# Kernel optimization log

Measured on AMD Instinct MI355X. Metric: run time of the kernel, lower is better.

Reference implementation:

```python
import jax, jax.numpy as jnp
import numpy as np

COMMITMENT_LOSS_WEIGHT = 0.25


def setup_inputs() -> dict:
    key = jax.random.key(0)
    k1, k2 = jax.random.split(key)
    B, H, W, C = 64, 32, 32, 256
    D, K = H * W, 1024  # embedding_dim = H*W per the rearrange+reshape in call()
    x = jax.random.normal(k1, (B, H, W, C), dtype=jnp.float32)
    # Orthogonal initializer (like tf.keras.initializers.Orthogonal) via QR
    E = jnp.linalg.qr(jax.random.normal(k2, (D, K), dtype=jnp.float32))[0]
    return {"x": x, "embeddings": E.astype(jnp.float32)}


def reference(x, embeddings):
    B, H, W, C = x.shape
    D = H * W  # embedding_dim
    # einops: 'b h w c -> b c (h w)'
    cont = jnp.transpose(x, (0, 3, 1, 2)).reshape(B, C, D)
    flat = cont.reshape(-1, D)  # [B*C, D]
    # squared L2 distances via norm + matmul (as in get_discretised)
    dists = (jnp.sum(flat * flat, axis=1, keepdims=True)
             + jnp.sum(embeddings * embeddings, axis=0)
             - 2.0 * (flat @ embeddings))  # [B*C, K]
    idx = jnp.argmin(dists, axis=1)  # [B*C]
    # one_hot @ embeddings.T == direct gather of codebook columns
    quantised = embeddings.T[idx].reshape(B, C, D)
    codebook_loss = jnp.mean((jax.lax.stop_gradient(cont) - quantised) ** 2)
    commitment_loss = COMMITMENT_LOSS_WEIGHT * jnp.mean(
        (cont - jax.lax.stop_gradient(quantised)) ** 2)
    loss = codebook_loss + commitment_loss  # layer add_loss terms, summed
    # einops: 'b c (h w) -> b h w c'
    q_bhwc = jnp.transpose(quantised.reshape(B, C, H, W), (0, 2, 3, 1))
    discretised = idx.reshape(-1, C)  # [B, C]
    # straight-through estimator
    q_out = x + jax.lax.stop_gradient(q_bhwc - x)
    return q_out, discretised, loss
```

## Files before the change

kernel.cpp:

```cpp
#include <hip/hip_runtime.h>
#include <float.h>
#include <stdint.h>

#define B_   64
#define C_   256
#define D_   1024
#define K_   1024
#define M_   16384
#define NX_  16777216
#define DISC_OFF NX_
#define LOSS_OFF (NX_ + M_)

typedef _Float16 h8 __attribute__((ext_vector_type(8)));
typedef float    f4 __attribute__((ext_vector_type(4)));

#define XSCALE 512.0f
#define ESCALE 2048.0f
#define DOT_UNSCALE_2 (2.0f / 1048576.0f)

#define WS_EH  0
#define WS_EL  524288
#define WS_CN  1048576
#define WS_PCN 1049600
#define WS_PV  1049600
#define WS_PI  1180672

__device__ __forceinline__ void async16(const _Float16* g, _Float16* l) {
    __builtin_amdgcn_global_load_lds(
        (const __attribute__((address_space(1))) unsigned int*)g,
        (__attribute__((address_space(3))) unsigned int*)l, 16, 0, 0);
}

__global__ __launch_bounds__(256) void split_kernel(const float* __restrict__ x,
                                                    const float* __restrict__ E,
                                                    _Float16* __restrict__ Xh,
                                                    _Float16* __restrict__ Xl,
                                                    _Float16* __restrict__ Eh,
                                                    _Float16* __restrict__ El,
                                                    float* __restrict__ pcn) {
    const int bid = blockIdx.x;
    if (bid < 512) {
        const int tid = bid * 256 + threadIdx.x;
        const int n   = tid & 1023;
        const int o   = tid >> 10;
        const int d0  = o * 8;
        h8 hh, ll;
        float s = 0.f;
        #pragma unroll
        for (int i = 0; i < 8; ++i) {
            const float v = E[(size_t)(d0 + i) * K_ + n];
            s = fmaf(v, v, s);
            const float vs = v * ESCALE;
            const _Float16 h = (_Float16)vs;
            hh[i] = h;
            ll[i] = (_Float16)(vs - (float)h);
        }
        pcn[o * K_ + n] = s;
        const int nt   = n >> 4;
        const int kt   = o >> 2;
        const int lane = (n & 15) + (o & 3) * 16;
        const size_t off = ((size_t)(nt * 32 + kt) * 64 + lane) * 8;
        *(h8*)(Eh + off) = hh;
        *(h8*)(El + off) = ll;
    } else {
        const int tid = (bid - 512) * 256 + threadIdx.x;
        const int m   = tid & 16383;
        const int o   = tid >> 14;
        const int b   = m >> 8, c = m & 255;
        const int d0  = o * 8;
        const float* xp = x + ((size_t)(b * 1024 + d0) * 256) + c;
        h8 hh, ll;
        #pragma unroll
        for (int i = 0; i < 8; ++i) {
            const float v  = xp[(size_t)i * 256];
            const float vs = v * XSCALE;
            const _Float16 h = (_Float16)vs;
            hh[i] = h;
            ll[i] = (_Float16)(vs - (float)h);
        }
        const int mt   = m >> 4;
        const int kt   = o >> 2;
        const int lane = (m & 15) + (o & 3) * 16;
        const size_t off = ((size_t)(mt * 32 + kt) * 64 + lane) * 8;
        *(h8*)(Xh + off) = hh;
        *(h8*)(Xl + off) = ll;
    }
}

__global__ __launch_bounds__(256) void colnorm2_kernel(const float* __restrict__ pcn,
                                                       float* __restrict__ cn,
                                                       float* __restrict__ loss_slot) {
    __shared__ float sp[4][64];
    const int t    = threadIdx.x;
    const int col  = blockIdx.x * 64 + (t & 63);
    const int part = t >> 6;
    float s = 0.f;
    #pragma unroll 8
    for (int i = 0; i < 32; ++i) s += pcn[(part * 32 + i) * K_ + col];
    sp[part][t & 63] = s;
    __syncthreads();
    if (t < 64) cn[col] = (sp[0][t] + sp[1][t]) + (sp[2][t] + sp[3][t]);
    if (blockIdx.x == 0 && t == 0) *loss_slot = 0.0f;
}

__global__ __launch_bounds__(512, 2) void gemm_argmin_kernel(
        const _Float16* __restrict__ Xh, const _Float16* __restrict__ Xl,
        const _Float16* __restrict__ Eh, const _Float16* __restrict__ El,
        const float* __restrict__ cn,
        float* __restrict__ pV, int* __restrict__ pI) {
    extern __shared__ _Float16 smem[];
    const int t    = threadIdx.x;
    const int bid  = blockIdx.x;
    const int swz  = (bid & 7) * 32 + (bid >> 3);
    const int rt   = swz >> 2;
    const int ct   = swz & 3;
    const int wave = t >> 6, lane = t & 63;
    const int lo16 = lane & 15, hi4 = lane >> 4;
    const int wr   = wave & 1, wc = wave >> 1;
    const int wr8  = wr * 8,  wc4 = wc * 4;
    const int mt0  = rt * 16, nt0 = ct * 16;
    const int n0g  = ct * 256;

    size_t gOff[4]; int lOff[4]; bool aFlag[4];
    #pragma unroll
    for (int i = 0; i < 4; ++i) {
        const int id = wave * 4 + i;
        if (id < 16) {
            aFlag[i] = true;
            gOff[i]  = (size_t)(mt0 + id) * 16384 + lane * 8;
            lOff[i]  = id * 512 + lane * 8;
        } else {
            aFlag[i] = false;
            gOff[i]  = (size_t)(nt0 + (id - 16)) * 16384 + lane * 8;
            lOff[i]  = 8192 + (id - 16) * 512 + lane * 8;
        }
    }

    f4 acc[8][4];
    const f4 zero = {0.f, 0.f, 0.f, 0.f};
    #pragma unroll
    for (int m = 0; m < 8; ++m)
        #pragma unroll
        for (int n = 0; n < 4; ++n) acc[m][n] = zero;

    auto stage = [&](int s2) {
        const int p  = s2 >> 5;
        const int kk = s2 & 31;
        const _Float16* Ab = (p < 2) ? Xh : Xl;
        const _Float16* Bb = (p == 1) ? El : Eh;
        _Float16* db = smem + (s2 & 3) * 16384;
        #pragma unroll
        for (int i = 0; i < 4; ++i)
            async16((aFlag[i] ? Ab : Bb) + gOff[i] + (size_t)kk * 512, db + lOff[i]);
    };

    auto body = [&](int s, bool doStage) {
        __builtin_amdgcn_s_barrier();
        asm volatile("" ::: "memory");
        if (doStage) stage(s + 3);
        const _Float16* rb = smem + (s & 3) * 16384;
        h8 Bf[4];
        #pragma unroll
        for (int n = 0; n < 4; ++n)
            Bf[n] = *(const h8*)(rb + 8192 + (wc4 + n) * 512 + lane * 8);
        __builtin_amdgcn_s_setprio(1);
        #pragma unroll
        for (int m = 0; m < 8; ++m) {
            const h8 Af = *(const h8*)(rb + (wr8 + m) * 512 + lane * 8);
            #pragma unroll
            for (int n = 0; n < 4; ++n)
                acc[m][n] = __builtin_amdgcn_mfma_f32_16x16x32_f16(Af, Bf[n], acc[m][n], 0, 0, 0);
        }
        __builtin_amdgcn_s_setprio(0);
    };

    stage(0); stage(1); stage(2);

    for (int s = 0; s < 94; ++s) {
        asm volatile("s_waitcnt vmcnt(8)" ::: "memory");
        body(s, s < 93);
    }
    asm volatile("s_waitcnt vmcnt(4)" ::: "memory");
    body(94, false);
    asm volatile("s_waitcnt vmcnt(0)" ::: "memory");
    body(95, false);

    __syncthreads();
    float* cV = (float*)smem;
    int*   cI = (int*)(cV + 1024);

    float cnv[4];
    #pragma unroll
    for (int n = 0; n < 4; ++n) cnv[n] = cn[n0g + wc * 64 + n * 16 + lo16];

    #pragma unroll
    for (int m = 0; m < 8; ++m) {
        #pragma unroll
        for (int r = 0; r < 4; ++r) {
            float bv = FLT_MAX;
            int   bi = 0;
            #pragma unroll
            for (int n = 0; n < 4; ++n) {
                const float v = cnv[n] - acc[m][n][r] * DOT_UNSCALE_2;
                if (v < bv) { bv = v; bi = wc * 64 + n * 16 + lo16; }
            }
            #pragma unroll
            for (int msk = 1; msk < 16; msk <<= 1) {
                const float ov = __shfl_xor(bv, msk, 64);
                const int   oi = __shfl_xor(bi, msk, 64);
                if (ov < bv || (ov == bv && oi < bi)) { bv = ov; bi = oi; }
            }
            if (lo16 == 0) {
                const int row = wr * 128 + m * 16 + hi4 * 4 + r;
                cV[row * 4 + wc] = bv;
                cI[row * 4 + wc] = bi;
            }
        }
    }
    __syncthreads();
    if (t < 256) {
        float bv = FLT_MAX;
        int   bi = 0;
        #pragma unroll
        for (int g = 0; g < 4; ++g) {
            const float v = cV[t * 4 + g];
            const int   i = cI[t * 4 + g];
            if (v < bv || (v == bv && i < bi)) { bv = v; bi = i; }
        }
        const int row = rt * 256 + t;
        pV[row * 4 + ct] = bv;
        pI[row * 4 + ct] = n0g + bi;
    }
}

__global__ __launch_bounds__(256) void reduce_kernel(const float* __restrict__ pV,
                                                     const int* __restrict__ pI,
                                                     float* __restrict__ disc) {
    const int rid = blockIdx.x * 256 + threadIdx.x;
    float bv = FLT_MAX;
    int   bi = 0;
    #pragma unroll
    for (int c = 0; c < 4; ++c) {
        const float v = pV[rid * 4 + c];
        const int   i = pI[rid * 4 + c];
        if (v < bv || (v == bv && i < bi)) { bv = v; bi = i; }
    }
    disc[rid] = (float)bi;
}

__global__ __launch_bounds__(256) void finalize_kernel(const float* __restrict__ x,
                                                       const float* __restrict__ E,
                                                       const float* __restrict__ discf,
                                                       float* __restrict__ out,
                                                       float* __restrict__ loss) {
    __shared__ float Erow[1024];
    const int t = threadIdx.x;
    const int d = blockIdx.x;
    *(float4*)&Erow[t * 4] = *(const float4*)(E + (size_t)d * K_ + t * 4);
    __syncthreads();

    const int bl = t >> 6;
    const int c4 = (t & 63) * 4;
    float lsum = 0.f;
    #pragma unroll 4
    for (int bg = 0; bg < 64; bg += 4) {
        const int b = bg + bl;
        const float4 id4 = *(const float4*)(discf + b * 256 + c4);
        const size_t xoff = ((size_t)(b * 1024 + d) << 8) + c4;
        const float4 xv = *(const float4*)(x + xoff);
        const float e0 = Erow[(int)id4.x];
        const float e1 = Erow[(int)id4.y];
        const float e2 = Erow[(int)id4.z];
        const float e3 = Erow[(int)id4.w];
        float4 qv;
        qv.x = xv.x + (e0 - xv.x);
        qv.y = xv.y + (e1 - xv.y);
        qv.z = xv.z + (e2 - xv.z);
        qv.w = xv.w + (e3 - xv.w);
        *(float4*)(out + xoff) = qv;
        const float d0 = xv.x - e0, d1 = xv.y - e1, d2 = xv.z - e2, d3 = xv.w - e3;
        lsum += fmaf(d0, d0, fmaf(d1, d1, fmaf(d2, d2, d3 * d3)));
    }

    #pragma unroll
    for (int off = 32; off > 0; off >>= 1)
        lsum += __shfl_down(lsum, off);
    __shared__ float wsum[4];
    if ((t & 63) == 0) wsum[t >> 6] = lsum;
    __syncthreads();
    if (t == 0) {
        const float s = (wsum[0] + wsum[1]) + (wsum[2] + wsum[3]);
        atomicAdd(loss, s * (1.25f / 16777216.0f));
    }
}

extern "C" void kernel_launch(void* const* d_in, const int* in_sizes, int n_in,
                              void* d_out, int out_size, void* d_ws, size_t ws_size,
                              hipStream_t stream) {
    (void)in_sizes; (void)n_in; (void)out_size; (void)ws_size;
    const float* x = (const float*)d_in[0];
    const float* E = (const float*)d_in[1];
    float* out = (float*)d_out;
    float* ws  = (float*)d_ws;

    _Float16* Eh = (_Float16*)(ws + WS_EH);
    _Float16* El = (_Float16*)(ws + WS_EL);
    float* cn    = ws + WS_CN;
    float* pcn   = ws + WS_PCN;
    float* pV    = ws + WS_PV;
    int*   pI    = (int*)(ws + WS_PI);

    _Float16* Xh = (_Float16*)out;
    _Float16* Xl = (_Float16*)out + NX_;
    float* disc  = out + DISC_OFF;
    float* loss  = out + LOSS_OFF;

    hipFuncSetAttribute((const void*)gemm_argmin_kernel,
                        hipFuncAttributeMaxDynamicSharedMemorySize, 131072);

    split_kernel   <<<8704, 256, 0, stream>>>(x, E, Xh, Xl, Eh, El, pcn);
    colnorm2_kernel<<<16,   256, 0, stream>>>(pcn, cn, loss);
    gemm_argmin_kernel<<<256, 512, 131072, stream>>>(Xh, Xl, Eh, El, cn, pV, pI);
    reduce_kernel  <<<64,   256, 0, stream>>>(pV, pI, disc);
    finalize_kernel<<<1024, 256, 0, stream>>>(x, E, disc, out, loss);
}
```

Baseline: 253.9 us.

## Use triple-buffered LDS pipeline with split staging interleaved between MFMA halves

The GEMM main loop goes from a 4-buffer, 3-stage-ahead prefetch to a 3-buffer, 2-stage-ahead prefetch. Each stage's global-to-LDS copies are split into two halves, issued between two half-batches of MFMAs. All LDS fragment reads are hoisted ahead of each MFMA batch with explicit lgkmcnt waits. Dynamic shared memory drops from 128 KB to 96 KB. The aim is to spread memory traffic across the compute phase, at the cost of a shallower prefetch that may expose more global load latency.

```diff
diff --git a/kernel.cpp b/kernel.cpp
--- a/kernel.cpp
+++ b/kernel.cpp
@@ -121,18 +121,18 @@
     const int mt0  = rt * 16, nt0 = ct * 16;
     const int n0g  = ct * 256;
 
-    size_t gOff[4]; int lOff[4]; bool aFlag[4];
+    size_t gOff[4]; int lOff[4]; bool isA[4];
     #pragma unroll
     for (int i = 0; i < 4; ++i) {
         const int id = wave * 4 + i;
         if (id < 16) {
-            aFlag[i] = true;
-            gOff[i]  = (size_t)(mt0 + id) * 16384 + lane * 8;
-            lOff[i]  = id * 512 + lane * 8;
+            isA[i] = true;
+            gOff[i] = (size_t)(mt0 + id) * 16384 + lane * 8;
+            lOff[i] = id * 512 + lane * 8;
         } else {
-            aFlag[i] = false;
-            gOff[i]  = (size_t)(nt0 + (id - 16)) * 16384 + lane * 8;
-            lOff[i]  = 8192 + (id - 16) * 512 + lane * 8;
+            isA[i] = false;
+            gOff[i] = (size_t)(nt0 + (id - 16)) * 16384 + lane * 8;
+            lOff[i] = 8192 + (id - 16) * 512 + lane * 8;
         }
     }
 
@@ -143,47 +143,61 @@
         #pragma unroll
         for (int n = 0; n < 4; ++n) acc[m][n] = zero;
 
-    auto stage = [&](int s2) {
+    auto stageHalf = [&](int s2, int half) {
         const int p  = s2 >> 5;
-        const int kk = s2 & 31;
-        const _Float16* Ab = (p < 2) ? Xh : Xl;
-        const _Float16* Bb = (p == 1) ? El : Eh;
-        _Float16* db = smem + (s2 & 3) * 16384;
-        #pragma unroll
-        for (int i = 0; i < 4; ++i)
-            async16((aFlag[i] ? Ab : Bb) + gOff[i] + (size_t)kk * 512, db + lOff[i]);
+        const int kt = s2 & 31;
+        const _Float16* Ap = (p < 2) ? Xh : Xl;
+        const _Float16* Bp = (p == 1) ? El : Eh;
+        _Float16* db = smem + (s2 % 3) * 16384;
+        #pragma unroll
+        for (int jj = 0; jj < 2; ++jj) {
+            const int i = half * 2 + jj;
+            async16((isA[i] ? Ap : Bp) + gOff[i] + (size_t)kt * 512, db + lOff[i]);
+        }
     };
 
-    auto body = [&](int s, bool doStage) {
+    auto step = [&](int s, bool doStage, bool last) {
+        if (last) { asm volatile("s_waitcnt vmcnt(0)" ::: "memory"); }
+        else      { asm volatile("s_waitcnt vmcnt(4)" ::: "memory"); }
         __builtin_amdgcn_s_barrier();
-        asm volatile("" ::: "memory");
-        if (doStage) stage(s + 3);
-        const _Float16* rb = smem + (s & 3) * 16384;
-        h8 Bf[4];
+        const _Float16* rb = smem + (s % 3) * 16384;
+        h8 Bf[4], Af[4];
         #pragma unroll
         for (int n = 0; n < 4; ++n)
             Bf[n] = *(const h8*)(rb + 8192 + (wc4 + n) * 512 + lane * 8);
+        #pragma unroll
+        for (int mm = 0; mm < 4; ++mm)
+            Af[mm] = *(const h8*)(rb + (wr8 + mm) * 512 + lane * 8);
+        if (doStage) stageHalf(s + 2, 0);
+        asm volatile("s_waitcnt lgkmcnt(0)" ::: "memory");
         __builtin_amdgcn_s_setprio(1);
         #pragma unroll
-        for (int m = 0; m < 8; ++m) {
-            const h8 Af = *(const h8*)(rb + (wr8 + m) * 512 + lane * 8);
+        for (int mm = 0; mm < 4; ++mm)
             #pragma unroll
             for (int n = 0; n < 4; ++n)
-                acc[m][n] = __builtin_amdgcn_mfma_f32_16x16x32_f16(Af, Bf[n], acc[m][n], 0, 0, 0);
-        }
+                acc[mm][n] = __builtin_amdgcn_mfma_f32_16x16x32_f16(Af[mm], Bf[n], acc[mm][n], 0, 0, 0);
+        __builtin_amdgcn_s_setprio(0);
+        h8 Ag[4];
+        #pragma unroll
+        for (int mm = 0; mm < 4; ++mm)
+            Ag[mm] = *(const h8*)(rb + (4 + wr8 + mm) * 512 + lane * 8);
+        if (doStage) stageHalf(s + 2, 1);
+        asm volatile("s_waitcnt lgkmcnt(0)" ::: "memory");
+        __builtin_amdgcn_s_setprio(1);
+        #pragma unroll
+        for (int mm = 0; mm < 4; ++mm)
+            #pragma unroll
+            for (int n = 0; n < 4; ++n)
+                acc[4 + mm][n] = __builtin_amdgcn_mfma_f32_16x16x32_f16(Ag[mm], Bf[n], acc[4 + mm][n], 0, 0, 0);
         __builtin_amdgcn_s_setprio(0);
     };
 
-    stage(0); stage(1); stage(2);
-
-    for (int s = 0; s < 94; ++s) {
-        asm volatile("s_waitcnt vmcnt(8)" ::: "memory");
-        body(s, s < 93);
-    }
-    asm volatile("s_waitcnt vmcnt(4)" ::: "memory");
-    body(94, false);
-    asm volatile("s_waitcnt vmcnt(0)" ::: "memory");
-    body(95, false);
+    stageHalf(0, 0); stageHalf(0, 1);
+    stageHalf(1, 0); stageHalf(1, 1);
+
+    for (int s = 0; s < 94; ++s) step(s, true, false);
+    step(94, false, false);
+    step(95, false, true);
 
     __syncthreads();
     float* cV = (float*)smem;
@@ -316,11 +330,11 @@
     float* loss  = out + LOSS_OFF;
 
     hipFuncSetAttribute((const void*)gemm_argmin_kernel,
-                        hipFuncAttributeMaxDynamicSharedMemorySize, 131072);
+                        hipFuncAttributeMaxDynamicSharedMemorySize, 98304);
 
     split_kernel   <<<8704, 256, 0, stream>>>(x, E, Xh, Xl, Eh, El, pcn);
     colnorm2_kernel<<<16,   256, 0, stream>>>(pcn, cn, loss);
-    gemm_argmin_kernel<<<256, 512, 131072, stream>>>(Xh, Xl, Eh, El, cn, pV, pI);
+    gemm_argmin_kernel<<<256, 512, 98304, stream>>>(Xh, Xl, Eh, El, cn, pV, pI);
     reduce_kernel  <<<64,   256, 0, stream>>>(pV, pI, disc);
     finalize_kernel<<<1024, 256, 0, stream>>>(x, E, disc, out, loss);
 }
```

After: 245.5 us. -3.3%, faster.
